# Optimization experiments

Hardware: AMD Instinct MI355X
Metric: run time of the kernel (lower is better)

The kernel has to match this reference:

```python
import jax, jax.numpy as jnp
import numpy as np
import math

B, S, HID = 2, 1024, 2048
NH, HD = 16, 128
STREAM_R, SELECT_R, RECENT_R = 0.02, 0.06, 0.08
FF = 0.9  # forgetting factor
ROPE_BASE = 10000.0


def setup_inputs() -> dict:
    key = jax.random.key(0)
    ks = jax.random.split(key, 5)
    return {
        "hidden_states": jax.random.normal(ks[0], (B, S, HID), dtype=jnp.float32),
        "wq": jax.random.normal(ks[1], (HID, HID), dtype=jnp.float32) * 0.02,
        "wk": jax.random.normal(ks[2], (HID, HID), dtype=jnp.float32) * 0.02,
        "wv": jax.random.normal(ks[3], (HID, HID), dtype=jnp.float32) * 0.02,
        "wo": jax.random.normal(ks[4], (HID, HID), dtype=jnp.float32) * 0.02,
    }


def _rope_tables(seq_len, dim):
    inv_freq = 1.0 / (ROPE_BASE ** (jnp.arange(0, dim, 2, dtype=jnp.float32) / dim))
    freqs = jnp.outer(jnp.arange(seq_len, dtype=jnp.float32), inv_freq)  # [S, D/2]
    emb = jnp.concatenate([freqs, freqs], axis=-1)  # [S, D]
    return jnp.cos(emb), jnp.sin(emb)


def _rotate_half(x):
    x1, x2 = jnp.split(x, 2, axis=-1)
    return jnp.concatenate([-x2, x1], axis=-1)


def a2s_base_mask(attn_weights, sb, selb, rb, ff):
    # attn_weights: [B,H,S,S] (causal mask already added). Returns bool keep-mask [B,H,S,S].
    Bv, Hv, Sq, Sk = attn_weights.shape
    scores = jax.nn.softmax(attn_weights.astype(jnp.float32), axis=-1)  # [B,H,S,S]
    cb = sb + selb + rb  # cache budget
    # EMA warmup over first cb rows: sum_i ff^(cb-1-i) * scores[i]
    w = ff ** jnp.arange(cb - 1, -1, -1, dtype=jnp.float32)
    select0 = jnp.einsum('t,bhts->bhs', w, scores[:, :, :cb, :])
    mask0 = jnp.ones((Bv, Hv, Sk), dtype=bool)
    pos = jnp.arange(Sk)

    xs_scores = jnp.moveaxis(scores[:, :, cb:Sk - 1, :], 2, 0)  # [T,B,H,S]
    ts = jnp.arange(cb, Sk - 1, dtype=jnp.int32)

    def step(carry, inp):
        sel, m = carry
        sc, t = inp
        cur = sc * m
        cur = cur / jnp.sum(cur, axis=-1, keepdims=True)
        sel = ff * sel + cur
        local = t - rb
        # argmin over window [sb : local+1]; outside -> +inf (evicted entries already +inf)
        win = jnp.where((pos >= sb) & (pos <= local), sel, jnp.inf)
        mi = jnp.argmin(win, axis=-1)  # [B,H], first-min like torch
        evict = pos == mi[..., None]  # [B,H,S] one-hot bool
        sel = jnp.where(evict, jnp.inf, sel)
        m_new = m & ~evict
        return (sel, m_new), m_new

    _, rows = jax.lax.scan(step, (select0, mask0), (xs_scores, ts))
    head = jnp.ones((Bv, Hv, cb + 1, Sk), dtype=bool)  # rows 0..cb stay all-True
    tail = jnp.moveaxis(rows, 0, 2)  # rows cb+1..S-1
    return jnp.concatenate([head, tail], axis=2)


def reference(hidden_states, wq, wk, wv, wo):
    sb = math.floor(STREAM_R * S + 0.5)
    selb = math.floor(SELECT_R * S + 0.5)
    rb = math.floor(RECENT_R * S + 0.5)

    q = (hidden_states @ wq).reshape(B, S, NH, HD).transpose(0, 2, 1, 3)
    k = (hidden_states @ wk).reshape(B, S, NH, HD).transpose(0, 2, 1, 3)
    v = (hidden_states @ wv).reshape(B, S, NH, HD).transpose(0, 2, 1, 3)

    cos, sin = _rope_tables(S, HD)  # [S,HD]
    q = q * cos + _rotate_half(q) * sin
    k = k * cos + _rotate_half(k) * sin

    attn = jnp.einsum('bhqd,bhkd->bhqk', q, k) / math.sqrt(HD)
    mask_val = jnp.finfo(jnp.float32).min
    causal = jnp.where(jnp.tril(jnp.ones((S, S), dtype=bool)), 0.0, mask_val)[None, None]
    attn = jnp.maximum(attn + causal, mask_val)

    keep = a2s_base_mask(jax.lax.stop_gradient(attn), sb, selb, rb, FF)
    attn = jnp.where(keep, attn, mask_val)  # torch.min(attention_mask) == mask_val

    probs = jax.nn.softmax(attn.astype(jnp.float32), axis=-1).astype(q.dtype)
    out = jnp.einsum('bhqk,bhkd->bhqd', probs, v)
    out = out.transpose(0, 2, 1, 3).reshape(B, S, HID)
    return out @ wo
```

## Files before the change

kernel.cpp:

```cpp
#include <hip/hip_runtime.h>
#include <math.h>

#define Bb    2
#define Ss    1024
#define HIDd  2048
#define NHh   16
#define HDd   128
#define SBc   20
#define SELBc 61
#define RBc   82
#define CBc   163
#define FFf   0.9f
#define MASKVAL (-3.4028234663852886e38f)
#define NBH   (Bb*NHh)
#define NROWS (NBH*Ss)

typedef __attribute__((ext_vector_type(8))) short short8;
typedef __attribute__((ext_vector_type(4))) float f32x4;

__device__ __forceinline__ unsigned short f2b(float f) {
    unsigned u = __float_as_uint(f);
    u = (u + 0x7FFFu + ((u >> 16) & 1u)) >> 16;
    return (unsigned short)u;
}
__device__ __forceinline__ float b2f(unsigned short h) {
    return __uint_as_float((unsigned)h << 16);
}

#if defined(__has_builtin)
#if __has_builtin(__builtin_amdgcn_global_load_lds)
#define USE_GLD 1
#endif
#endif

__device__ __forceinline__ void gload16(const void* g, void* l) {
#ifdef USE_GLD
    __builtin_amdgcn_global_load_lds(
        (const __attribute__((address_space(1))) void*)g,
        (__attribute__((address_space(3))) void*)l, 16, 0, 0);
#else
    *(short8*)l = *(const short8*)g;
#endif
}

__global__ __launch_bounds__(256) void conv_split(const float* __restrict__ x,
                                                  unsigned short* __restrict__ yh,
                                                  unsigned short* __restrict__ yl, int n4)
{
    int i = blockIdx.x * 256 + threadIdx.x;
    if (i >= n4) return;
    float4 v = ((const float4*)x)[i];
    ushort4 h, l;
    h.x = f2b(v.x); l.x = f2b(v.x - b2f(h.x));
    h.y = f2b(v.y); l.y = f2b(v.y - b2f(h.y));
    h.z = f2b(v.z); l.z = f2b(v.z - b2f(h.z));
    h.w = f2b(v.w); l.w = f2b(v.w - b2f(h.w));
    ((ushort4*)yh)[i] = h;
    ((ushort4*)yl)[i] = l;
}

__global__ __launch_bounds__(256) void tconv_all(const float* __restrict__ wq,
                                                 const float* __restrict__ wk,
                                                 const float* __restrict__ wv,
                                                 const float* __restrict__ wo,
                                                 unsigned short* __restrict__ wqth,
                                                 unsigned short* __restrict__ wqtl,
                                                 unsigned short* __restrict__ wkth,
                                                 unsigned short* __restrict__ wktl,
                                                 unsigned short* __restrict__ wvt,
                                                 unsigned short* __restrict__ wot)
{
    __shared__ float T[64][65];
    const int z = blockIdx.z;
    const float* W = (z == 0) ? wq : (z == 1) ? wk : (z == 2) ? wv : wo;
    int n0 = blockIdx.x * 64, k0 = blockIdx.y * 64;
    int tid = threadIdx.x;
    int rr = tid >> 4, cc = (tid & 15) * 4;
#pragma unroll
    for (int p = 0; p < 4; ++p) {
        int r = rr + p * 16;
        float4 x = *(const float4*)&W[(size_t)(k0 + r) * HIDd + n0 + cc];
        T[r][cc] = x.x; T[r][cc + 1] = x.y; T[r][cc + 2] = x.z; T[r][cc + 3] = x.w;
    }
    __syncthreads();
    if (z < 2) {
        unsigned short* Wth = z ? wkth : wqth;
        unsigned short* Wtl = z ? wktl : wqtl;
#pragma unroll
        for (int p = 0; p < 4; ++p) {
            int rn = rr + p * 16;
            float v0 = T[cc][rn], v1 = T[cc + 1][rn], v2 = T[cc + 2][rn], v3 = T[cc + 3][rn];
            ushort4 h, l;
            h.x = f2b(v0); l.x = f2b(v0 - b2f(h.x));
            h.y = f2b(v1); l.y = f2b(v1 - b2f(h.y));
            h.z = f2b(v2); l.z = f2b(v2 - b2f(h.z));
            h.w = f2b(v3); l.w = f2b(v3 - b2f(h.w));
            *(ushort4*)&Wth[(size_t)(n0 + rn) * HIDd + k0 + cc] = h;
            *(ushort4*)&Wtl[(size_t)(n0 + rn) * HIDd + k0 + cc] = l;
        }
    } else {
        unsigned short* Wt = (z == 2) ? wvt : wot;
#pragma unroll
        for (int p = 0; p < 4; ++p) {
            int rn = rr + p * 16;
            ushort4 o;
            o.x = f2b(T[cc][rn]);     o.y = f2b(T[cc + 1][rn]);
            o.z = f2b(T[cc + 2][rn]); o.w = f2b(T[cc + 3][rn]);
            *(ushort4*)&Wt[(size_t)(n0 + rn) * HIDd + k0 + cc] = o;
        }
    }
}

__global__ __launch_bounds__(256) void gemm_qkv(const unsigned short* __restrict__ hsh,
                                                const unsigned short* __restrict__ hsl,
                                                const unsigned short* __restrict__ wqth,
                                                const unsigned short* __restrict__ wqtl,
                                                const unsigned short* __restrict__ wkth,
                                                const unsigned short* __restrict__ wktl,
                                                const unsigned short* __restrict__ wvt,
                                                float* __restrict__ qf,
                                                float* __restrict__ kf,
                                                float* __restrict__ vf)
{
    __shared__ unsigned short AsH[128 * 32], AsL[128 * 32];
    __shared__ unsigned short BsH[128 * 32], BsL[128 * 32];
    const int tid = threadIdx.x;
    const int region = blockIdx.x >> 4;
    const int bn = (blockIdx.x & 15) * 128;
    const int bm = blockIdx.y * 128;
    const int K = HIDd;
    const int lane = tid & 63, wid = tid >> 6;
    const int wr = (wid >> 1) * 64, wc = (wid & 1) * 64;
    const int lm = lane & 15, lk = (lane >> 4) * 8;
    const int lr = (lane >> 4) * 4;

    f32x4 acc[4][4];
#pragma unroll
    for (int mi = 0; mi < 4; ++mi)
#pragma unroll
        for (int ni = 0; ni < 4; ++ni) acc[mi][ni] = 0.0f;

    if (region < 2) {
        const unsigned short* Bh = region ? wkth : wqth;
        const unsigned short* Bl = region ? wktl : wqtl;
        float* C = region ? kf : qf;
        for (int k0 = 0; k0 < K; k0 += 32) {
#pragma unroll
            for (int l = 0; l < 2; ++l) {
                int L = tid + l * 256;
                int row = L >> 2, c8 = (L & 3) * 8;
                size_t ga = (size_t)(bm + row) * K + k0 + c8;
                size_t gb = (size_t)(bn + row) * K + k0 + c8;
                gload16(&hsh[ga], &AsH[L * 8]);
                gload16(&hsl[ga], &AsL[L * 8]);
                gload16(&Bh[gb], &BsH[L * 8]);
                gload16(&Bl[gb], &BsL[L * 8]);
            }
            __syncthreads();
            short8 ah[4], al[4], bh[4], bl[4];
#pragma unroll
            for (int mi = 0; mi < 4; ++mi) {
                ah[mi] = *(short8*)&AsH[(wr + mi * 16 + lm) * 32 + lk];
                al[mi] = *(short8*)&AsL[(wr + mi * 16 + lm) * 32 + lk];
            }
#pragma unroll
            for (int ni = 0; ni < 4; ++ni) {
                bh[ni] = *(short8*)&BsH[(wc + ni * 16 + lm) * 32 + lk];
                bl[ni] = *(short8*)&BsL[(wc + ni * 16 + lm) * 32 + lk];
            }
#pragma unroll
            for (int mi = 0; mi < 4; ++mi)
#pragma unroll
                for (int ni = 0; ni < 4; ++ni) {
                    acc[mi][ni] = __builtin_amdgcn_mfma_f32_16x16x32_bf16(ah[mi], bh[ni], acc[mi][ni], 0, 0, 0);
                    acc[mi][ni] = __builtin_amdgcn_mfma_f32_16x16x32_bf16(ah[mi], bl[ni], acc[mi][ni], 0, 0, 0);
                    acc[mi][ni] = __builtin_amdgcn_mfma_f32_16x16x32_bf16(al[mi], bh[ni], acc[mi][ni], 0, 0, 0);
                }
            __syncthreads();
        }
#pragma unroll
        for (int mi = 0; mi < 4; ++mi)
#pragma unroll
            for (int ni = 0; ni < 4; ++ni)
#pragma unroll
                for (int r = 0; r < 4; ++r) {
                    int m = bm + wr + mi * 16 + lr + r;
                    int n = bn + wc + ni * 16 + lm;
                    int b_ = m / Ss, s_ = m % Ss;
                    int h_ = n / HDd, d_ = n % HDd;
                    C[(size_t)((b_ * NHh + h_) * Ss + s_) * HDd + d_] = acc[mi][ni][r];
                }
    } else {
        for (int k0 = 0; k0 < K; k0 += 32) {
#pragma unroll
            for (int l = 0; l < 2; ++l) {
                int L = tid + l * 256;
                int row = L >> 2, c8 = (L & 3) * 8;
                gload16(&hsh[(size_t)(bm + row) * K + k0 + c8], &AsH[L * 8]);
                gload16(&wvt[(size_t)(bn + row) * K + k0 + c8], &BsH[L * 8]);
            }
            __syncthreads();
            short8 af[4], bf[4];
#pragma unroll
            for (int mi = 0; mi < 4; ++mi) af[mi] = *(short8*)&AsH[(wr + mi * 16 + lm) * 32 + lk];
#pragma unroll
            for (int ni = 0; ni < 4; ++ni) bf[ni] = *(short8*)&BsH[(wc + ni * 16 + lm) * 32 + lk];
#pragma unroll
            for (int mi = 0; mi < 4; ++mi)
#pragma unroll
                for (int ni = 0; ni < 4; ++ni)
                    acc[mi][ni] = __builtin_amdgcn_mfma_f32_16x16x32_bf16(af[mi], bf[ni], acc[mi][ni], 0, 0, 0);
            __syncthreads();
        }
#pragma unroll
        for (int mi = 0; mi < 4; ++mi)
#pragma unroll
            for (int ni = 0; ni < 4; ++ni)
#pragma unroll
                for (int r = 0; r < 4; ++r) {
                    int m = bm + wr + mi * 16 + lr + r;
                    int n = bn + wc + ni * 16 + lm;
                    int b_ = m / Ss, s_ = m % Ss;
                    int h_ = n / HDd, d_ = n % HDd;
                    vf[(size_t)((b_ * NHh + h_) * Ss + s_) * HDd + d_] = acc[mi][ni][r];
                }
    }
}

__global__ __launch_bounds__(256) void gemm_bf16t(const unsigned short* __restrict__ A,
                                                  const unsigned short* __restrict__ Bt,
                                                  float* __restrict__ C,
                                                  int M, int N, int K)
{
    __shared__ unsigned short As[128 * 32];
    __shared__ unsigned short Bs[64 * 32];
    const int tid = threadIdx.x;
    const int bm = blockIdx.y * 128, bn = blockIdx.x * 64;
    const int lane = tid & 63, wid = tid >> 6;
    const int wr = (wid >> 1) * 64, wc = (wid & 1) * 32;
    const int lm = lane & 15, lk = (lane >> 4) * 8;

    f32x4 acc[4][2];
#pragma unroll
    for (int mi = 0; mi < 4; ++mi)
#pragma unroll
        for (int ni = 0; ni < 2; ++ni) acc[mi][ni] = 0.0f;

    for (int k0 = 0; k0 < K; k0 += 32) {
#pragma unroll
        for (int l = 0; l < 2; ++l) {
            int L = tid + l * 256;
            int row = L >> 2, c8 = (L & 3) * 8;
            gload16(&A[(size_t)(bm + row) * K + k0 + c8], &As[L * 8]);
        }
        {
            int row = tid >> 2, c8 = (tid & 3) * 8;
            gload16(&Bt[(size_t)(bn + row) * K + k0 + c8], &Bs[tid * 8]);
        }
        __syncthreads();
        short8 af[4], bf[2];
#pragma unroll
        for (int mi = 0; mi < 4; ++mi) af[mi] = *(short8*)&As[(wr + mi * 16 + lm) * 32 + lk];
#pragma unroll
        for (int ni = 0; ni < 2; ++ni) bf[ni] = *(short8*)&Bs[(wc + ni * 16 + lm) * 32 + lk];
#pragma unroll
        for (int mi = 0; mi < 4; ++mi)
#pragma unroll
            for (int ni = 0; ni < 2; ++ni)
                acc[mi][ni] = __builtin_amdgcn_mfma_f32_16x16x32_bf16(af[mi], bf[ni], acc[mi][ni], 0, 0, 0);
        __syncthreads();
    }
    const int lr = (lane >> 4) * 4;
#pragma unroll
    for (int mi = 0; mi < 4; ++mi)
#pragma unroll
        for (int ni = 0; ni < 2; ++ni)
#pragma unroll
            for (int r = 0; r < 4; ++r) {
                int m = bm + wr + mi * 16 + lr + r;
                int n = bn + wc + ni * 16 + lm;
                C[(size_t)m * N + n] = acc[mi][ni][r];
            }
}

__global__ __launch_bounds__(64) void rope_qk_split(const float* __restrict__ q,
                                                    const float* __restrict__ k,
                                                    unsigned short* __restrict__ qh,
                                                    unsigned short* __restrict__ ql,
                                                    unsigned short* __restrict__ kh,
                                                    unsigned short* __restrict__ kl)
{
    int idx = blockIdx.x;
    int s = idx % Ss;
    int d = threadIdx.x;
    float inv = powf(10000.0f, -2.0f * (float)d / 128.0f);
    float fr = (float)s * inv;
    float c = cosf(fr), sn = sinf(fr);
    size_t base = (size_t)idx * HDd;
    float q1 = q[base + d], q2 = q[base + d + 64];
    float k1 = k[base + d], k2 = k[base + d + 64];
    float qa = q1 * c - q2 * sn, qbv = q2 * c + q1 * sn;
    float ka = k1 * c - k2 * sn, kbv = k2 * c + k1 * sn;
    unsigned short h;
    h = f2b(qa);  qh[base + d]      = h; ql[base + d]      = f2b(qa  - b2f(h));
    h = f2b(qbv); qh[base + d + 64] = h; ql[base + d + 64] = f2b(qbv - b2f(h));
    h = f2b(ka);  kh[base + d]      = h; kl[base + d]      = f2b(ka  - b2f(h));
    h = f2b(kbv); kh[base + d + 64] = h; kl[base + d + 64] = f2b(kbv - b2f(h));
}

__global__ __launch_bounds__(256) void attn_qk_split(const unsigned short* __restrict__ qh,
                                                     const unsigned short* __restrict__ ql,
                                                     const unsigned short* __restrict__ kh,
                                                     const unsigned short* __restrict__ kl,
                                                     float* __restrict__ attn)
{
    const int bh = blockIdx.z;
    const int bm = blockIdx.y * 128, bn = blockIdx.x * 128;
    const int tid = threadIdx.x;

    if (blockIdx.x > blockIdx.y) return;
    const bool diag = (blockIdx.x == blockIdx.y);

    float* C = attn + (size_t)bh * Ss * Ss;
    const size_t hb = (size_t)bh * Ss * HDd;
    const unsigned short* Ah = qh + hb;
    const unsigned short* Al = ql + hb;
    const unsigned short* Bh = kh + hb;
    const unsigned short* Bl = kl + hb;

    __shared__ unsigned short AsH[128 * 32], AsL[128 * 32];
    __shared__ unsigned short BsH[128 * 32], BsL[128 * 32];
    const int lane = tid & 63, wid = tid >> 6;
    const int wr = (wid >> 1) * 64, wc = (wid & 1) * 64;
    const int lm = lane & 15, lk = (lane >> 4) * 8;

    f32x4 acc[4][4];
#pragma unroll
    for (int mi = 0; mi < 4; ++mi)
#pragma unroll
        for (int ni = 0; ni < 4; ++ni) acc[mi][ni] = 0.0f;

    for (int k0 = 0; k0 < HDd; k0 += 32) {
#pragma unroll
        for (int l = 0; l < 2; ++l) {
            int L = tid + l * 256;
            int row = L >> 2, c8 = (L & 3) * 8;
            size_t ga = (size_t)(bm + row) * HDd + k0 + c8;
            size_t gb = (size_t)(bn + row) * HDd + k0 + c8;
            gload16(&Ah[ga], &AsH[L * 8]);
            gload16(&Al[ga], &AsL[L * 8]);
            gload16(&Bh[gb], &BsH[L * 8]);
            gload16(&Bl[gb], &BsL[L * 8]);
        }
        __syncthreads();
        short8 ah[4], al[4], bh2[4], bl2[4];
#pragma unroll
        for (int mi = 0; mi < 4; ++mi) {
            ah[mi] = *(short8*)&AsH[(wr + mi * 16 + lm) * 32 + lk];
            al[mi] = *(short8*)&AsL[(wr + mi * 16 + lm) * 32 + lk];
        }
#pragma unroll
        for (int ni = 0; ni < 4; ++ni) {
            bh2[ni] = *(short8*)&BsH[(wc + ni * 16 + lm) * 32 + lk];
            bl2[ni] = *(short8*)&BsL[(wc + ni * 16 + lm) * 32 + lk];
        }
#pragma unroll
        for (int mi = 0; mi < 4; ++mi)
#pragma unroll
            for (int ni = 0; ni < 4; ++ni) {
                if (diag && (wc + ni * 16 > wr + mi * 16 + 15)) continue;
                acc[mi][ni] = __builtin_amdgcn_mfma_f32_16x16x32_bf16(ah[mi], bh2[ni], acc[mi][ni], 0, 0, 0);
                acc[mi][ni] = __builtin_amdgcn_mfma_f32_16x16x32_bf16(ah[mi], bl2[ni], acc[mi][ni], 0, 0, 0);
                acc[mi][ni] = __builtin_amdgcn_mfma_f32_16x16x32_bf16(al[mi], bh2[ni], acc[mi][ni], 0, 0, 0);
            }
        __syncthreads();
    }
    const float scale = 0.08838834764831845f;
    const int lr = (lane >> 4) * 4;
#pragma unroll
    for (int mi = 0; mi < 4; ++mi)
#pragma unroll
        for (int ni = 0; ni < 4; ++ni)
#pragma unroll
            for (int r = 0; r < 4; ++r) {
                int sq = bm + wr + mi * 16 + lr + r;
                int sk = bn + wc + ni * 16 + lm;
                C[(size_t)sq * Ss + sk] = (sk <= sq) ? acc[mi][ni][r] * scale : MASKVAL;
            }
}

__global__ __launch_bounds__(256) void softmax_rows(float* __restrict__ attn)
{
    int row = blockIdx.x;
    int r = row & (Ss - 1);
    float4* a4 = (float4*)(attn + (size_t)row * Ss);
    int tid = threadIdx.x;
    bool act = (tid * 4 <= r);
    float4 x = make_float4(MASKVAL, MASKVAL, MASKVAL, MASKVAL);
    if (act) x = a4[tid];
    float m = fmaxf(fmaxf(x.x, x.y), fmaxf(x.z, x.w));
#pragma unroll
    for (int off = 32; off; off >>= 1) m = fmaxf(m, __shfl_xor(m, off));
    __shared__ float red[4];
    if ((tid & 63) == 0) red[tid >> 6] = m;
    __syncthreads();
    float mm = fmaxf(fmaxf(red[0], red[1]), fmaxf(red[2], red[3]));
    float e0 = expf(x.x - mm), e1 = expf(x.y - mm);
    float e2 = expf(x.z - mm), e3 = expf(x.w - mm);
    float s = e0 + e1 + e2 + e3;
#pragma unroll
    for (int off = 32; off; off >>= 1) s += __shfl_xor(s, off);
    __shared__ float red2[4];
    if ((tid & 63) == 0) red2[tid >> 6] = s;
    __syncthreads();
    float inv = 1.0f / (red2[0] + red2[1] + red2[2] + red2[3]);
    a4[tid] = make_float4(e0 * inv, e1 * inv, e2 * inv, e3 * inv);
}

template<int CTRL>
__device__ __forceinline__ int dpp_i(int x) {
    return __builtin_amdgcn_update_dpp(0, x, CTRL, 0xF, 0xF, true);
}
__device__ __forceinline__ float wave_sum64(float x) {
    x += __int_as_float(dpp_i<0xB1>(__float_as_int(x)));
    x += __int_as_float(dpp_i<0x4E>(__float_as_int(x)));
    x += __int_as_float(dpp_i<0x141>(__float_as_int(x)));
    x += __int_as_float(dpp_i<0x140>(__float_as_int(x)));
    int xi = __float_as_int(x);
    float a = __int_as_float(__builtin_amdgcn_readlane(xi, 0));
    float b = __int_as_float(__builtin_amdgcn_readlane(xi, 16));
    float c = __int_as_float(__builtin_amdgcn_readlane(xi, 32));
    float d = __int_as_float(__builtin_amdgcn_readlane(xi, 48));
    return (a + c) + (b + d);
}

__device__ __forceinline__ unsigned long long u64min(unsigned long long a, unsigned long long b) {
    return a < b ? a : b;
}
template<int CTRL>
__device__ __forceinline__ unsigned long long dpp64(unsigned long long x) {
    int lo = (int)(unsigned)x;
    int hi = (int)(unsigned)(x >> 32);
    unsigned l2 = (unsigned)dpp_i<CTRL>(lo);
    unsigned h2 = (unsigned)dpp_i<CTRL>(hi);
    return ((unsigned long long)h2 << 32) | (unsigned long long)l2;
}
__device__ __forceinline__ unsigned long long wave_min64k(unsigned long long x) {
    x = u64min(x, dpp64<0xB1>(x));
    x = u64min(x, dpp64<0x4E>(x));
    x = u64min(x, dpp64<0x141>(x));
    x = u64min(x, dpp64<0x140>(x));
    int lo = (int)(unsigned)x;
    int hi = (int)(unsigned)(x >> 32);
    unsigned long long a = ((unsigned long long)(unsigned)__builtin_amdgcn_readlane(hi, 0)  << 32) |
                           (unsigned long long)(unsigned)__builtin_amdgcn_readlane(lo, 0);
    unsigned long long b = ((unsigned long long)(unsigned)__builtin_amdgcn_readlane(hi, 16) << 32) |
                           (unsigned long long)(unsigned)__builtin_amdgcn_readlane(lo, 16);
    unsigned long long c = ((unsigned long long)(unsigned)__builtin_amdgcn_readlane(hi, 32) << 32) |
                           (unsigned long long)(unsigned)__builtin_amdgcn_readlane(lo, 32);
    unsigned long long d = ((unsigned long long)(unsigned)__builtin_amdgcn_readlane(hi, 48) << 32) |
                           (unsigned long long)(unsigned)__builtin_amdgcn_readlane(lo, 48);
    return u64min(u64min(a, b), u64min(c, d));
}

__device__ __forceinline__ float f4c(float4 v, int i) {
    return i == 0 ? v.x : (i == 1 ? v.y : (i == 2 ? v.z : v.w));
}

template<int NC, int NCL>
__device__ __forceinline__ void scan_step(int t, int lane,
                                          const float4* __restrict__ A4,
                                          unsigned char* __restrict__ KP,
                                          float4 (&rb)[4],
                                          float (&sel)[4][4],
                                          float (&mf)[4][4])
{
    const float INFv = __int_as_float(0x7f800000);
    float4 a[NC];
#pragma unroll
    for (int jj = 0; jj < NC; ++jj) a[jj] = rb[jj];
    int tp = t + 4; if (tp > Ss - 1) tp = Ss - 1;
#pragma unroll
    for (int jj = 0; jj < NCL; ++jj) rb[jj] = A4[tp * 256 + jj * 64 + lane];

    float lsum = 0.0f;
#pragma unroll
    for (int jj = 0; jj < NC; ++jj) {
        float c0 = a[jj].x * mf[jj][0], c1 = a[jj].y * mf[jj][1];
        float c2 = a[jj].z * mf[jj][2], c3 = a[jj].w * mf[jj][3];
        lsum += (c0 + c1) + (c2 + c3);
    }
    float tot = wave_sum64(lsum);
    float inv = 1.0f / tot;

    const int local = t - RBc;
    const int base = lane * 4;
    const bool ge = (base >= SBc);

    unsigned long long kmin = 0xFFFFFFFFFFFFFFFFull;
#pragma unroll
    for (int jj = 0; jj < NC; ++jj) {
        unsigned long long kk[4];
#pragma unroll
        for (int i = 0; i < 4; ++i) {
            float sv = fmaf(FFf, sel[jj][i], f4c(a[jj], i) * inv);
            sel[jj][i] = sv;
            int s = jj * 256 + base + i;
            bool win = (s <= local) && (jj > 0 || ge);
            unsigned hi = win ? __float_as_uint(sv) : 0x7f800000u;
            kk[i] = ((unsigned long long)hi << 32) | (unsigned long long)(unsigned)s;
        }
        unsigned long long cm = u64min(u64min(kk[0], kk[1]), u64min(kk[2], kk[3]));
        kmin = u64min(kmin, cm);
    }
    kmin = wave_min64k(kmin);
    const int besti = (int)(unsigned)(kmin & 0xFFFFFFFFull);

#pragma unroll
    for (int jj = 0; jj < NC; ++jj)
#pragma unroll
        for (int i = 0; i < 4; ++i) {
            int s = jj * 256 + base + i;
            bool e = (s == besti);
            sel[jj][i] = e ? INFv : sel[jj][i];
            mf[jj][i]  = e ? 0.0f : mf[jj][i];
        }

    uchar4* kp4 = (uchar4*)(KP + (size_t)(t + 1) * Ss);
#pragma unroll
    for (int jj = 0; jj < NC; ++jj) {
        uchar4 kb;
        kb.x = (unsigned char)mf[jj][0];
        kb.y = (unsigned char)mf[jj][1];
        kb.z = (unsigned char)mf[jj][2];
        kb.w = (unsigned char)mf[jj][3];
        kp4[jj * 64 + lane] = kb;
    }
}

__global__ __launch_bounds__(64) void scan_kernel5(const float* __restrict__ scores,
                                                   unsigned char* __restrict__ keep)
{
    int bh = blockIdx.x;
    int lane = threadIdx.x;
    const float4* A4 = (const float4*)(scores + (size_t)bh * Ss * Ss);
    unsigned char* KP = keep + (size_t)bh * Ss * Ss;

    float sel[4][4];
    float mf[4][4];
#pragma unroll
    for (int jj = 0; jj < 4; ++jj)
#pragma unroll
        for (int i = 0; i < 4; ++i) { sel[jj][i] = 0.0f; mf[jj][i] = 1.0f; }

    float4 w0 = A4[0 * 256 + lane];
    float4 w1 = A4[1 * 256 + lane];
    float4 w2 = A4[2 * 256 + lane];
    float4 w3 = A4[3 * 256 + lane];
#define WSTEP(W, NEXT)                                                       \
    do {                                                                     \
        float4 _a = W;                                                       \
        W = A4[(NEXT) * 256 + lane];                                         \
        sel[0][0] = fmaf(FFf, sel[0][0], _a.x);                              \
        sel[0][1] = fmaf(FFf, sel[0][1], _a.y);                              \
        sel[0][2] = fmaf(FFf, sel[0][2], _a.z);                              \
        sel[0][3] = fmaf(FFf, sel[0][3], _a.w);                              \
    } while (0)
    for (int r = 0; r < 160; r += 4) {
        WSTEP(w0, r + 4); WSTEP(w1, r + 5); WSTEP(w2, r + 6); WSTEP(w3, r + 7);
    }
#undef WSTEP
    {
        float4 tl[3] = { w0, w1, w2 };
#pragma unroll
        for (int u = 0; u < 3; ++u) {
            sel[0][0] = fmaf(FFf, sel[0][0], tl[u].x);
            sel[0][1] = fmaf(FFf, sel[0][1], tl[u].y);
            sel[0][2] = fmaf(FFf, sel[0][2], tl[u].z);
            sel[0][3] = fmaf(FFf, sel[0][3], tl[u].w);
        }
    }

    float4 rb[4][4];
#pragma unroll
    for (int slot = 0; slot < 4; ++slot)
        rb[slot][0] = A4[(163 + slot) * 256 + lane];

    for (int t0 = 163; t0 < 255; t0 += 4) {
        scan_step<1, 2>(t0 + 0, lane, A4, KP, rb[0], sel, mf);
        scan_step<1, 2>(t0 + 1, lane, A4, KP, rb[1], sel, mf);
        scan_step<1, 2>(t0 + 2, lane, A4, KP, rb[2], sel, mf);
        scan_step<1, 2>(t0 + 3, lane, A4, KP, rb[3], sel, mf);
    }
    for (int t0 = 255; t0 < 511; t0 += 4) {
        scan_step<2, 3>(t0 + 0, lane, A4, KP, rb[0], sel, mf);
        scan_step<2, 3>(t0 + 1, lane, A4, KP, rb[1], sel, mf);
        scan_step<2, 3>(t0 + 2, lane, A4, KP, rb[2], sel, mf);
        scan_step<2, 3>(t0 + 3, lane, A4, KP, rb[3], sel, mf);
    }
    for (int t0 = 511; t0 < 767; t0 += 4) {
        scan_step<3, 4>(t0 + 0, lane, A4, KP, rb[0], sel, mf);
        scan_step<3, 4>(t0 + 1, lane, A4, KP, rb[1], sel, mf);
        scan_step<3, 4>(t0 + 2, lane, A4, KP, rb[2], sel, mf);
        scan_step<3, 4>(t0 + 3, lane, A4, KP, rb[3], sel, mf);
    }
    for (int t0 = 767; t0 < 1023; t0 += 4) {
        scan_step<4, 4>(t0 + 0, lane, A4, KP, rb[0], sel, mf);
        scan_step<4, 4>(t0 + 1, lane, A4, KP, rb[1], sel, mf);
        scan_step<4, 4>(t0 + 2, lane, A4, KP, rb[2], sel, mf);
        scan_step<4, 4>(t0 + 3, lane, A4, KP, rb[3], sel, mf);
    }
}

__global__ __launch_bounds__(256) void pv_renorm(const float* __restrict__ scores,
                                                 const unsigned char* __restrict__ keep,
                                                 const float* __restrict__ v,
                                                 unsigned short* __restrict__ ctxb)
{
    int bh = blockIdx.z;
    int b_ = bh / NHh, h_ = bh % NHh;
    const float* P = scores + (size_t)bh * Ss * Ss;
    const unsigned char* KPm = keep + (size_t)bh * Ss * Ss;
    const float* V = v + (size_t)bh * Ss * HDd;
    int bm = blockIdx.y * 64, bn = blockIdx.x * 64;
    int tid = threadIdx.x, tx = tid & 15, ty = tid >> 4;
    __shared__ float As[16][68];
    __shared__ float Bs[16][64];
    float acc[4][4] = {};
    float rs[4] = {};
    int kend = bm + 64;
    for (int k0 = 0; k0 < kend; k0 += 16) {
#pragma unroll
        for (int l = 0; l < 4; ++l) {
            int idx = tid + l * 256;
            int r = idx >> 4, c = idx & 15;
            int row = bm + r;
            float p = P[(size_t)row * Ss + k0 + c];
            if (row > CBc && !KPm[(size_t)row * Ss + k0 + c]) p = 0.0f;
            As[c][r] = p;
        }
#pragma unroll
        for (int l = 0; l < 4; ++l) {
            int idx = tid + l * 256;
            int r = idx >> 6, c = idx & 63;
            Bs[r][c] = V[(size_t)(k0 + r) * HDd + bn + c];
        }
        __syncthreads();
#pragma unroll
        for (int kk = 0; kk < 16; ++kk) {
            float4 av = *(const float4*)&As[kk][ty * 4];
            float4 bv = *(const float4*)&Bs[kk][tx * 4];
            float a[4] = { av.x, av.y, av.z, av.w };
            float b[4] = { bv.x, bv.y, bv.z, bv.w };
#pragma unroll
            for (int i = 0; i < 4; ++i) rs[i] += a[i];
#pragma unroll
            for (int i = 0; i < 4; ++i)
#pragma unroll
                for (int j = 0; j < 4; ++j)
                    acc[i][j] = fmaf(a[i], b[j], acc[i][j]);
        }
        __syncthreads();
    }
#pragma unroll
    for (int i = 0; i < 4; ++i) {
        float inv = 1.0f / rs[i];
        int sq = bm + ty * 4 + i;
#pragma unroll
        for (int j = 0; j < 4; ++j) {
            int d = bn + tx * 4 + j;
            ctxb[(size_t)(b_ * Ss + sq) * HIDd + h_ * HDd + d] = f2b(acc[i][j] * inv);
        }
    }
}

extern "C" void kernel_launch(void* const* d_in, const int* in_sizes, int n_in,
                              void* d_out, int out_size, void* d_ws, size_t ws_size,
                              hipStream_t stream)
{
    const float* hs = (const float*)d_in[0];
    const float* wq = (const float*)d_in[1];
    const float* wk = (const float*)d_in[2];
    const float* wv = (const float*)d_in[3];
    const float* wo = (const float*)d_in[4];
    float* out = (float*)d_out;

    float* ws = (float*)d_ws;
    size_t off = 0;
    float* qf   = ws + off; off += (size_t)NBH * Ss * HDd;
    float* kf   = ws + off; off += (size_t)NBH * Ss * HDd;
    float* vf   = ws + off; off += (size_t)NBH * Ss * HDd;
    float* attn = ws + off; off += (size_t)NBH * Ss * Ss;
    unsigned char* keep = (unsigned char*)(ws + off); off += (size_t)NBH * Ss * Ss / 4;
    unsigned short* wot = (unsigned short*)(ws + off); off += (size_t)HIDd * HIDd / 2;

    unsigned short* hsh  = (unsigned short*)(attn);
    unsigned short* hsl  = (unsigned short*)(attn + 2u * 1024 * 1024);
    unsigned short* wqth = (unsigned short*)(attn + 4u * 1024 * 1024);
    unsigned short* wqtl = (unsigned short*)(attn + 6u * 1024 * 1024);
    unsigned short* wkth = (unsigned short*)(attn + 8u * 1024 * 1024);
    unsigned short* wktl = (unsigned short*)(attn + 10u * 1024 * 1024);
    unsigned short* wvt  = (unsigned short*)(attn + 12u * 1024 * 1024);
    unsigned short* qh = (unsigned short*)keep;
    unsigned short* ql = (unsigned short*)(keep + 8u * 1024 * 1024);
    unsigned short* kh = (unsigned short*)(keep + 16u * 1024 * 1024);
    unsigned short* kl = (unsigned short*)(keep + 24u * 1024 * 1024);
    unsigned short* ctxb = (unsigned short*)qf;

    dim3 blk(256);
    const int M = Bb * Ss;

    conv_split<<<dim3((M * HIDd / 4 + 255) / 256), blk, 0, stream>>>(hs, hsh, hsl, M * HIDd / 4);

    tconv_all<<<dim3(HIDd / 64, HIDd / 64, 4), blk, 0, stream>>>(
        wq, wk, wv, wo, wqth, wqtl, wkth, wktl, wvt, wot);

    gemm_qkv<<<dim3(48, M / 128), blk, 0, stream>>>(
        hsh, hsl, wqth, wqtl, wkth, wktl, wvt, qf, kf, vf);

    rope_qk_split<<<dim3(NBH * Ss), dim3(64), 0, stream>>>(qf, kf, qh, ql, kh, kl);

    attn_qk_split<<<dim3(Ss / 128, Ss / 128, NBH), blk, 0, stream>>>(qh, ql, kh, kl, attn);

    softmax_rows<<<dim3(NROWS), blk, 0, stream>>>(attn);

    scan_kernel5<<<dim3(NBH), dim3(64), 0, stream>>>(attn, keep);

    pv_renorm<<<dim3(HDd / 64, Ss / 64, NBH), blk, 0, stream>>>(attn, keep, vf, ctxb);

    gemm_bf16t<<<dim3(HIDd / 64, M / 128), blk, 0, stream>>>(ctxb, wot, out, M, HIDd, HIDd);
}
```

Measured before the change: 969.1 us.

## Move PV product to split-bf16 MFMA with transposed V

Replaces the scalar fp32 FMA probs×V kernel with an MFMA kernel that splits masked probabilities and V into bf16 hi/lo pairs and accumulates three cross products. Row sums are computed with MFMA against a ones vector. A new transpose kernel writes V as hi/lo bf16 in d-major layout into the freed K buffer. This aims to cut the ALU cost of the PV stage, at the price of an extra launch, more memory traffic for V, and a small loss of precision from the split-bf16 approximation.

```diff
diff --git a/kernel.cpp b/kernel.cpp
--- a/kernel.cpp
+++ b/kernel.cpp
@@ -108,6 +108,38 @@
             o.z = f2b(T[cc + 2][rn]); o.w = f2b(T[cc + 3][rn]);
             *(ushort4*)&Wt[(size_t)(n0 + rn) * HIDd + k0 + cc] = o;
         }
+    }
+}
+
+__global__ __launch_bounds__(256) void vtrans(const float* __restrict__ vf,
+                                              unsigned short* __restrict__ vth,
+                                              unsigned short* __restrict__ vtl)
+{
+    __shared__ float T[64][65];
+    const int bh = blockIdx.z;
+    int d0 = blockIdx.x * 64, s0 = blockIdx.y * 64;
+    int tid = threadIdx.x;
+    int rr = tid >> 4, cc = (tid & 15) * 4;
+    const float* V = vf + (size_t)bh * Ss * HDd;
+#pragma unroll
+    for (int p = 0; p < 4; ++p) {
+        int r = rr + p * 16;
+        float4 x = *(const float4*)&V[(size_t)(s0 + r) * HDd + d0 + cc];
+        T[r][cc] = x.x; T[r][cc + 1] = x.y; T[r][cc + 2] = x.z; T[r][cc + 3] = x.w;
+    }
+    __syncthreads();
+#pragma unroll
+    for (int p = 0; p < 4; ++p) {
+        int rn = rr + p * 16;
+        float v0 = T[cc][rn], v1 = T[cc + 1][rn], v2 = T[cc + 2][rn], v3 = T[cc + 3][rn];
+        ushort4 h, l;
+        h.x = f2b(v0); l.x = f2b(v0 - b2f(h.x));
+        h.y = f2b(v1); l.y = f2b(v1 - b2f(h.y));
+        h.z = f2b(v2); l.z = f2b(v2 - b2f(h.z));
+        h.w = f2b(v3); l.w = f2b(v3 - b2f(h.w));
+        size_t ob = ((size_t)bh * HDd + d0 + rn) * Ss + s0 + cc;
+        *(ushort4*)&vth[ob] = h;
+        *(ushort4*)&vtl[ob] = l;
     }
 }
 
@@ -612,66 +644,109 @@
     }
 }
 
-__global__ __launch_bounds__(256) void pv_renorm(const float* __restrict__ scores,
-                                                 const unsigned char* __restrict__ keep,
-                                                 const float* __restrict__ v,
-                                                 unsigned short* __restrict__ ctxb)
-{
-    int bh = blockIdx.z;
-    int b_ = bh / NHh, h_ = bh % NHh;
+__global__ __launch_bounds__(256) void pv_mfma(const float* __restrict__ scores,
+                                               const unsigned char* __restrict__ keep,
+                                               const unsigned short* __restrict__ vth,
+                                               const unsigned short* __restrict__ vtl,
+                                               unsigned short* __restrict__ ctxb)
+{
+    __shared__ unsigned short AsH[128 * 32], AsL[128 * 32];
+    __shared__ unsigned short BsH[64 * 32],  BsL[64 * 32];
+    const int bh = blockIdx.z;
+    const int b_ = bh / NHh, h_ = bh % NHh;
     const float* P = scores + (size_t)bh * Ss * Ss;
     const unsigned char* KPm = keep + (size_t)bh * Ss * Ss;
-    const float* V = v + (size_t)bh * Ss * HDd;
-    int bm = blockIdx.y * 64, bn = blockIdx.x * 64;
-    int tid = threadIdx.x, tx = tid & 15, ty = tid >> 4;
-    __shared__ float As[16][68];
-    __shared__ float Bs[16][64];
-    float acc[4][4] = {};
-    float rs[4] = {};
-    int kend = bm + 64;
-    for (int k0 = 0; k0 < kend; k0 += 16) {
+    const unsigned short* Vh = vth + (size_t)bh * HDd * Ss;
+    const unsigned short* Vl = vtl + (size_t)bh * HDd * Ss;
+    const int bm = blockIdx.y * 128, bn = blockIdx.x * 64;
+    const int tid = threadIdx.x;
+    const int lane = tid & 63, wid = tid >> 6;
+    const int wr = (wid >> 1) * 64, wc = (wid & 1) * 32;
+    const int lm = lane & 15, lk = (lane >> 4) * 8;
+
+    short8 ones;
+#pragma unroll
+    for (int i = 0; i < 8; ++i) ones[i] = (short)0x3F80;
+
+    f32x4 acc[4][2];
+    f32x4 rsa[4];
+#pragma unroll
+    for (int mi = 0; mi < 4; ++mi) {
+        rsa[mi] = 0.0f;
+#pragma unroll
+        for (int ni = 0; ni < 2; ++ni) acc[mi][ni] = 0.0f;
+    }
+
+    const int kend = bm + 128;
+    for (int k0 = 0; k0 < kend; k0 += 32) {
 #pragma unroll
         for (int l = 0; l < 4; ++l) {
             int idx = tid + l * 256;
-            int r = idx >> 4, c = idx & 15;
-            int row = bm + r;
-            float p = P[(size_t)row * Ss + k0 + c];
-            if (row > CBc && !KPm[(size_t)row * Ss + k0 + c]) p = 0.0f;
-            As[c][r] = p;
-        }
-#pragma unroll
-        for (int l = 0; l < 4; ++l) {
+            int row = idx >> 3, c4 = (idx & 7) * 4;
+            size_t ga = (size_t)(bm + row) * Ss + k0 + c4;
+            float4 p4 = *(const float4*)&P[ga];
+            if (bm + row > CBc) {
+                uchar4 kb = *(const uchar4*)&KPm[ga];
+                if (!kb.x) p4.x = 0.0f;
+                if (!kb.y) p4.y = 0.0f;
+                if (!kb.z) p4.z = 0.0f;
+                if (!kb.w) p4.w = 0.0f;
+            }
+            ushort4 h, l2;
+            h.x = f2b(p4.x); l2.x = f2b(p4.x - b2f(h.x));
+            h.y = f2b(p4.y); l2.y = f2b(p4.y - b2f(h.y));
+            h.z = f2b(p4.z); l2.z = f2b(p4.z - b2f(h.z));
+            h.w = f2b(p4.w); l2.w = f2b(p4.w - b2f(h.w));
+            *(ushort4*)&AsH[row * 32 + c4] = h;
+            *(ushort4*)&AsL[row * 32 + c4] = l2;
+        }
+#pragma unroll
+        for (int l = 0; l < 2; ++l) {
             int idx = tid + l * 256;
-            int r = idx >> 6, c = idx & 63;
-            Bs[r][c] = V[(size_t)(k0 + r) * HDd + bn + c];
+            int row = idx >> 3, c4 = (idx & 7) * 4;
+            size_t gb = (size_t)(bn + row) * Ss + k0 + c4;
+            *(ushort4*)&BsH[row * 32 + c4] = *(const ushort4*)&Vh[gb];
+            *(ushort4*)&BsL[row * 32 + c4] = *(const ushort4*)&Vl[gb];
         }
         __syncthreads();
-#pragma unroll
-        for (int kk = 0; kk < 16; ++kk) {
-            float4 av = *(const float4*)&As[kk][ty * 4];
-            float4 bv = *(const float4*)&Bs[kk][tx * 4];
-            float a[4] = { av.x, av.y, av.z, av.w };
-            float b[4] = { bv.x, bv.y, bv.z, bv.w };
-#pragma unroll
-            for (int i = 0; i < 4; ++i) rs[i] += a[i];
-#pragma unroll
-            for (int i = 0; i < 4; ++i)
-#pragma unroll
-                for (int j = 0; j < 4; ++j)
-                    acc[i][j] = fmaf(a[i], b[j], acc[i][j]);
+        short8 ah[4], al[4], bhf[2], blf[2];
+#pragma unroll
+        for (int mi = 0; mi < 4; ++mi) {
+            ah[mi] = *(short8*)&AsH[(wr + mi * 16 + lm) * 32 + lk];
+            al[mi] = *(short8*)&AsL[(wr + mi * 16 + lm) * 32 + lk];
+        }
+#pragma unroll
+        for (int ni = 0; ni < 2; ++ni) {
+            bhf[ni] = *(short8*)&BsH[(wc + ni * 16 + lm) * 32 + lk];
+            blf[ni] = *(short8*)&BsL[(wc + ni * 16 + lm) * 32 + lk];
+        }
+#pragma unroll
+        for (int mi = 0; mi < 4; ++mi) {
+            rsa[mi] = __builtin_amdgcn_mfma_f32_16x16x32_bf16(ah[mi], ones, rsa[mi], 0, 0, 0);
+            rsa[mi] = __builtin_amdgcn_mfma_f32_16x16x32_bf16(al[mi], ones, rsa[mi], 0, 0, 0);
+#pragma unroll
+            for (int ni = 0; ni < 2; ++ni) {
+                acc[mi][ni] = __builtin_amdgcn_mfma_f32_16x16x32_bf16(ah[mi], bhf[ni], acc[mi][ni], 0, 0, 0);
+                acc[mi][ni] = __builtin_amdgcn_mfma_f32_16x16x32_bf16(ah[mi], blf[ni], acc[mi][ni], 0, 0, 0);
+                acc[mi][ni] = __builtin_amdgcn_mfma_f32_16x16x32_bf16(al[mi], bhf[ni], acc[mi][ni], 0, 0, 0);
+            }
         }
         __syncthreads();
     }
-#pragma unroll
-    for (int i = 0; i < 4; ++i) {
-        float inv = 1.0f / rs[i];
-        int sq = bm + ty * 4 + i;
-#pragma unroll
-        for (int j = 0; j < 4; ++j) {
-            int d = bn + tx * 4 + j;
-            ctxb[(size_t)(b_ * Ss + sq) * HIDd + h_ * HDd + d] = f2b(acc[i][j] * inv);
-        }
-    }
+    const int lr = (lane >> 4) * 4;
+#pragma unroll
+    for (int mi = 0; mi < 4; ++mi)
+#pragma unroll
+        for (int r = 0; r < 4; ++r) {
+            int sq = bm + wr + mi * 16 + lr + r;
+            float inv = 1.0f / rsa[mi][r];
+            size_t ob = (size_t)(b_ * Ss + sq) * HIDd + h_ * HDd;
+#pragma unroll
+            for (int ni = 0; ni < 2; ++ni) {
+                int d = bn + wc + ni * 16 + lm;
+                ctxb[ob + d] = f2b(acc[mi][ni][r] * inv);
+            }
+        }
 }
 
 extern "C" void kernel_launch(void* const* d_in, const int* in_sizes, int n_in,
@@ -705,6 +780,8 @@
     unsigned short* ql = (unsigned short*)(keep + 8u * 1024 * 1024);
     unsigned short* kh = (unsigned short*)(keep + 16u * 1024 * 1024);
     unsigned short* kl = (unsigned short*)(keep + 24u * 1024 * 1024);
+    unsigned short* vth = (unsigned short*)kf;
+    unsigned short* vtl = (unsigned short*)kf + (size_t)NBH * HDd * Ss;
     unsigned short* ctxb = (unsigned short*)qf;
 
     dim3 blk(256);
@@ -720,13 +797,15 @@
 
     rope_qk_split<<<dim3(NBH * Ss), dim3(64), 0, stream>>>(qf, kf, qh, ql, kh, kl);
 
+    vtrans<<<dim3(HDd / 64, Ss / 64, NBH), blk, 0, stream>>>(vf, vth, vtl);
+
     attn_qk_split<<<dim3(Ss / 128, Ss / 128, NBH), blk, 0, stream>>>(qh, ql, kh, kl, attn);
 
     softmax_rows<<<dim3(NROWS), blk, 0, stream>>>(attn);
 
     scan_kernel5<<<dim3(NBH), dim3(64), 0, stream>>>(attn, keep);
 
-    pv_renorm<<<dim3(HDd / 64, Ss / 64, NBH), blk, 0, stream>>>(attn, keep, vf, ctxb);
+    pv_mfma<<<dim3(HDd / 64, Ss / 128, NBH), blk, 0, stream>>>(attn, keep, vth, vtl, ctxb);
 
     gemm_bf16t<<<dim3(HIDd / 64, M / 128), blk, 0, stream>>>(ctxb, wot, out, M, HIDd, HIDd);
 }
```

After: 903.8 us. 6.7% less time.
